# Optimization experiments

Hardware: AMD Instinct MI355X
Metric: run time of the kernel (lower is better)

The kernel has to match this reference:

```python
import jax, jax.numpy as jnp
import numpy as np

B, S, HID, H = 8, 128, 256, 4
DH = HID // H
FF = 4 * HID


def setup_inputs() -> dict:
    key = jax.random.key(0)
    ks = jax.random.split(key, 16)
    n = lambda i, shape: jax.random.normal(ks[i], shape, dtype=jnp.float32) * 0.02
    z = lambda shape: jnp.zeros(shape, dtype=jnp.float32)
    return dict(
        x=jax.random.normal(ks[0], (B, S, HID), dtype=jnp.float32),
        attention_mask=jnp.zeros((B, 1, S, S), dtype=jnp.float32),
        Wq=n(1, (HID, HID)), bq=z((HID,)),
        Wk=n(2, (HID, HID)), bk=z((HID,)),
        Wv=n(3, (HID, HID)), bv=z((HID,)),
        order_w=n(4, (2 * DH,)), order_b=z(()),
        dist_w=n(5, (2 * DH,)), dist_b=z(()),
        scalar=jax.random.normal(ks[6], (1,), dtype=jnp.float32),
        AWq=n(7, (HID, HID)), Abq=z((HID,)),
        AWk=n(8, (HID, HID)), Abk=z((HID,)),
        Wd=n(9, (HID, HID)), bd=z((HID,)),
        g1=jnp.ones((HID,), jnp.float32), beta1=z((HID,)),
        W1=n(10, (HID, FF)), b1=z((FF,)),
        W2=n(11, (FF, HID)), b2=z((HID,)),
        g2=jnp.ones((HID,), jnp.float32), beta2=z((HID,)),
    )


def _ln(t, g, b, eps=1e-12):
    m = t.mean(-1, keepdims=True)
    v = ((t - m) ** 2).mean(-1, keepdims=True)
    return (t - m) / jnp.sqrt(v + eps) * g + b


def _heads(t):
    # [B,S,HID] -> [B,H,S,DH]
    return t.reshape(B, S, H, DH).transpose(0, 2, 1, 3)


def reference(x, attention_mask, Wq, bq, Wk, bk, Wv, bv, order_w, order_b,
              dist_w, dist_b, scalar, AWq, Abq, AWk, Abk, Wd, bd,
              g1, beta1, W1, b1, W2, b2, g2, beta2):
    inv = 1.0 / jnp.sqrt(jnp.float32(DH))
    q = x @ Wq + bq
    k = x @ Wk + bk
    v = x @ Wv + bv
    qh, kh, vh = _heads(q), _heads(k), _heads(v)
    scores = jnp.einsum('bhqd,bhkd->bhqk', qh, kh)  # [B,H,S,S]

    # order/distance affines on concat(q_i, k_j): Linear(2*DH,1) decomposes into
    # per-token projections summed via broadcast (same math, no [B,H,S,S,2*DH] tensor)
    pr_order = jax.nn.sigmoid((qh @ order_w[:DH])[..., :, None]
                              + (kh @ order_w[DH:])[..., None, :] + order_b)
    gd_order = jnp.triu(jnp.ones((S, S), jnp.float32), k=1)
    err_order = (jnp.log(pr_order + 1e-24) * gd_order
                 + jnp.log(1.0 - pr_order + 1e-24) * (1.0 - gd_order))

    idx = jnp.arange(S)
    gd_dist = jnp.log(jnp.abs(idx[None, :] - idx[:, None]).astype(jnp.float32) + 1.0)
    pr_dist = ((qh @ dist_w[:DH])[..., :, None]
               + (kh @ dist_w[DH:])[..., None, :] + dist_b)
    err_dist = -jnp.square(gd_dist - pr_dist) * jnp.square(scalar[0]) * 0.5

    rich_scores = scores + err_order + err_dist
    softm = lambda s: jax.nn.softmax(s * inv + attention_mask, axis=-1)
    rich_probs = softm(rich_scores)
    origin_probs = softm(scores)

    # rich/calibrated combine ('fixed'): softmax(origin + 0.5 * rich)
    combined = jax.nn.softmax(origin_probs + 0.5 * rich_probs, axis=-1)

    # two-level attack attention on transformed mixed q/k
    aq, ak = _heads(q @ AWq + Abq), _heads(k @ AWk + Abk)
    attack_probs = softm(jnp.einsum('bhqd,bhkd->bhqk', aq, ak))
    final_probs = jax.nn.softmax(combined + 0.5 * attack_probs, axis=-1)

    ctx = jnp.einsum('bhqk,bhkd->bhqd', final_probs, vh)
    ctx = ctx.transpose(0, 2, 1, 3).reshape(B, S, HID)
    h = _ln(ctx @ Wd + bd + x, g1, beta1)
    f = jax.nn.gelu(h @ W1 + b1, approximate=False) @ W2 + b2
    return _ln(f + h, g2, beta2)
```

## Files before the change

kernel.cpp:

```cpp
#include <hip/hip_runtime.h>
#include <math.h>

#define B_  8
#define S_  128
#define HID_ 256
#define H_  4
#define DH_ 64
#define FF_ 1024
#define M_  (B_ * S_)

typedef _Float16 half_t;
typedef __attribute__((ext_vector_type(8))) _Float16 half8;
typedef __attribute__((ext_vector_type(4))) float floatx4;

enum { EP_F32 = 0, EP_F16 = 1, EP_F16B = 2, EP_GELU = 3, EP_PROJ = 4 };

__device__ __forceinline__ floatx4 mfma16(half8 a, half8 b, floatx4 c) {
    return __builtin_amdgcn_mfma_f32_16x16x32_f16(a, b, c, 0, 0, 0);
}

__device__ __forceinline__ float qred_sum(float v) {
#pragma unroll
    for (int o = 1; o < 16; o <<= 1) v += __shfl_xor(v, o, 64);
    return v;
}
__device__ __forceinline__ float wred64(float v) {
#pragma unroll
    for (int o = 1; o < 64; o <<= 1) v += __shfl_xor(v, o, 64);
    return v;
}
__device__ __forceinline__ void sm8(float (&v)[8]) {
    float s = 0.f;
#pragma unroll
    for (int j = 0; j < 8; ++j) { v[j] = __expf(v[j]); s += v[j]; }
    s = qred_sum(s);
    float r = 1.f / s;
#pragma unroll
    for (int j = 0; j < 8; ++j) v[j] *= r;
}

template<int EPI, int KLEN>
__device__ __forceinline__ void mgemm(
    half8 (&Asf)[2][4][64], half8 (&Bsf)[2][4][64],
    const half_t* __restrict__ A, int ldA,
    const half_t* __restrict__ Bt, int ldB,
    int m0, int n0,
    const float* __restrict__ bias,
    float* __restrict__ Cf, half_t* __restrict__ Ch, int ldC,
    const float* __restrict__ pw1, const float* __restrict__ pw2,
    float* __restrict__ po1, float* __restrict__ po2, int hsel,
    int tidp)
{
    constexpr int kt = KLEN >> 5;
    const int w = tidp >> 6, l = tidp & 63;
    const int sr = tidp >> 2;
    const int sq = tidp & 3;
    const int sdst = (sr & 15) | (sq << 4);
    const int smt = sr >> 4;
    const half_t* Ap = A + (size_t)(m0 + sr) * ldA + sq * 8;
    const half_t* Bp = Bt + (size_t)(n0 + sr) * ldB + sq * 8;

    half8 ra[kt], rb[kt];
#pragma unroll
    for (int t = 0; t < kt; ++t) {
        ra[t] = *(const half8*)(Ap + t * 32);
        rb[t] = *(const half8*)(Bp + t * 32);
    }

    floatx4 zero = {0.f, 0.f, 0.f, 0.f};
    floatx4 acc[4] = {zero, zero, zero, zero};

    Asf[0][smt][sdst] = ra[0];
    Bsf[0][smt][sdst] = rb[0];
    __syncthreads();
#pragma unroll
    for (int t = 0; t < kt; ++t) {
        const int buf = t & 1;
        half8 a = Asf[buf][w][l];
        acc[0] = mfma16(a, Bsf[buf][0][l], acc[0]);
        acc[1] = mfma16(a, Bsf[buf][1][l], acc[1]);
        acc[2] = mfma16(a, Bsf[buf][2][l], acc[2]);
        acc[3] = mfma16(a, Bsf[buf][3][l], acc[3]);
        if (t + 1 < kt) {
            Asf[buf ^ 1][smt][sdst] = ra[t + 1];
            Bsf[buf ^ 1][smt][sdst] = rb[t + 1];
            __syncthreads();
        }
    }

    const int quad = l >> 4, lc = l & 15;
    const int rowb = m0 + w * 16 + quad * 4;
    float bvv[4] = {0.f, 0.f, 0.f, 0.f};
    if (EPI >= EP_F16B) {
#pragma unroll
        for (int nt = 0; nt < 4; ++nt) bvv[nt] = bias[n0 + nt * 16 + lc];
    }
    float pw1v[4], pw2v[4];
    if (EPI == EP_PROJ) {
#pragma unroll
        for (int nt = 0; nt < 4; ++nt) {
            pw1v[nt] = pw1[nt * 16 + lc];
            pw2v[nt] = pw2[nt * 16 + lc];
        }
    }
#pragma unroll
    for (int rr = 0; rr < 4; ++rr) {
        float ov[4];
#pragma unroll
        for (int nt = 0; nt < 4; ++nt) {
            float o = acc[nt][rr];
            if (EPI >= EP_F16B) o += bvv[nt];
            if (EPI == EP_GELU) o = 0.5f * o * (1.f + erff(o * 0.70710678118654752f));
            ov[nt] = o;
            const size_t ci = (size_t)(rowb + rr) * ldC + n0 + nt * 16 + lc;
            if (EPI == EP_F32) Cf[ci] = o;
            else Ch[ci] = (half_t)o;
        }
        if (EPI == EP_PROJ) {
            float po = ov[0] * pw1v[0] + ov[1] * pw1v[1] + ov[2] * pw1v[2] + ov[3] * pw1v[3];
            float pd = ov[0] * pw2v[0] + ov[1] * pw2v[1] + ov[2] * pw2v[2] + ov[3] * pw2v[3];
#pragma unroll
            for (int off = 1; off < 16; off <<= 1) {
                po += __shfl_xor(po, off, 64);
                pd += __shfl_xor(pd, off, 64);
            }
            if (lc == 0) {
                const int m = rowb + rr;
                const int idx = ((m >> 7) * H_ + hsel) * S_ + (m & 127);
                po1[idx] = po;
                po2[idx] = pd;
            }
        }
    }
}

__global__ __launch_bounds__(256) void prep_kernel(
    const float* __restrict__ x,
    const float* __restrict__ Wq, const float* __restrict__ Wk,
    const float* __restrict__ Wv, const float* __restrict__ Wd,
    const float* __restrict__ W1, const float* __restrict__ W2,
    const float* __restrict__ AWq, const float* __restrict__ AWk,
    const float* __restrict__ bq, const float* __restrict__ bk,
    const float* __restrict__ Abq, const float* __restrict__ Abk,
    half_t* __restrict__ x16, half_t* __restrict__ WqT, half_t* __restrict__ WkT,
    half_t* __restrict__ WvT, half_t* __restrict__ WdT,
    half_t* __restrict__ W1T, half_t* __restrict__ W2T,
    half_t* __restrict__ WcqT, half_t* __restrict__ WckT,
    float* __restrict__ bcq, float* __restrict__ bck)
{
    __shared__ union {
        half_t tl[64][72];
        struct { half_t As[64][264]; half_t Bs[64][264]; } c;
        float red[4][64];
    } sm;
    const int tid = threadIdx.x;
    const int j = blockIdx.x;

    if (j < 256) {
        const int base = j * 1024 + tid * 4;
        float4 vv = *(const float4*)(x + base);
        x16[base + 0] = (half_t)vv.x;
        x16[base + 1] = (half_t)vv.y;
        x16[base + 2] = (half_t)vv.z;
        x16[base + 3] = (half_t)vv.w;
        return;
    }
    if (j < 448) {
        int t = j - 256;
        const float* src; half_t* dst; int K, N, k0, n0;
        if (t < 64) {
            int m = t >> 4, q = t & 15;
            const float* ins[4] = {Wq, Wk, Wv, Wd};
            half_t* outs[4] = {WqT, WkT, WvT, WdT};
            src = ins[m]; dst = outs[m]; K = 256; N = 256;
            k0 = (q & 3) * 64; n0 = (q >> 2) * 64;
        } else if (t < 128) {
            int q = t - 64; src = W1; dst = W1T; K = 256; N = 1024;
            k0 = (q & 3) * 64; n0 = (q >> 2) * 64;
        } else {
            int q = t - 128; src = W2; dst = W2T; K = 1024; N = 256;
            k0 = (q >> 2) * 64; n0 = (q & 3) * 64;
        }
        const int r = tid >> 2, c0 = (tid & 3) * 16;
#pragma unroll 4
        for (int i = 0; i < 16; ++i)
            sm.tl[c0 + i][r] = (half_t)src[(size_t)(k0 + r) * N + n0 + c0 + i];
        __syncthreads();
#pragma unroll 4
        for (int i = 0; i < 16; ++i)
            dst[(size_t)(n0 + r) * K + k0 + c0 + i] = sm.tl[r][c0 + i];
        return;
    }
    if (j < 480) {
        int t = j - 448;
        const int z = t >> 4, q = t & 15;
        const int m0 = (q >> 2) * 64, n0 = (q & 3) * 64;
        const float* AW = z ? AWk : AWq;
        const float* W  = z ? Wk : Wq;
        half_t* C       = z ? WckT : WcqT;
        {
            const float* srcA = AW + (size_t)tid * HID_ + m0;
#pragma unroll 4
            for (int i = 0; i < 16; ++i) {
                float4 v = *(const float4*)(srcA + i * 4);
                sm.c.As[i * 4 + 0][tid] = (half_t)v.x;
                sm.c.As[i * 4 + 1][tid] = (half_t)v.y;
                sm.c.As[i * 4 + 2][tid] = (half_t)v.z;
                sm.c.As[i * 4 + 3][tid] = (half_t)v.w;
            }
        }
        {
            const int bn = tid >> 2, bc = (tid & 3) * 64;
            const float* srcB = W + (size_t)(n0 + bn) * HID_ + bc;
            half_t* dstB = &sm.c.Bs[bn][bc];
#pragma unroll 4
            for (int i = 0; i < 16; ++i) {
                float4 v = *(const float4*)(srcB + i * 4);
                dstB[i * 4 + 0] = (half_t)v.x;
                dstB[i * 4 + 1] = (half_t)v.y;
                dstB[i * 4 + 2] = (half_t)v.z;
                dstB[i * 4 + 3] = (half_t)v.w;
            }
        }
        __syncthreads();
        const int w = tid >> 6, l = tid & 63;
        const int quad = l >> 4, lc = l & 15;
        const floatx4 zero = {0.f, 0.f, 0.f, 0.f};
        floatx4 acc[4] = {zero, zero, zero, zero};
#pragma unroll
        for (int kt = 0; kt < 8; ++kt) {
            half8 a = *(const half8*)&sm.c.As[w * 16 + lc][kt * 32 + quad * 8];
#pragma unroll
            for (int nt = 0; nt < 4; ++nt) {
                half8 b = *(const half8*)&sm.c.Bs[nt * 16 + lc][kt * 32 + quad * 8];
                acc[nt] = mfma16(a, b, acc[nt]);
            }
        }
#pragma unroll
        for (int nt = 0; nt < 4; ++nt)
#pragma unroll
            for (int rr = 0; rr < 4; ++rr)
                C[(size_t)(m0 + w * 16 + quad * 4 + rr) * HID_ + n0 + nt * 16 + lc] =
                    (half_t)acc[nt][rr];
        return;
    }
    {
        int t = j - 480;
        const int z = t >> 2, xb = t & 3;
        const float* bsrc = z ? bk : bq;
        const float* AW   = z ? AWk : AWq;
        const float* Ab   = z ? Abk : Abq;
        float* bco        = z ? bck : bcq;
        int l = tid & 63, kc = tid >> 6;
        int n = xb * 64 + l;
        float p = 0.f;
#pragma unroll 8
        for (int kk = 0; kk < 64; ++kk) {
            int k = kc * 64 + kk;
            p = fmaf(bsrc[k], AW[(size_t)k * HID_ + n], p);
        }
        sm.red[kc][l] = p;
        __syncthreads();
        if (kc == 0)
            bco[n] = sm.red[0][l] + sm.red[1][l] + sm.red[2][l] + sm.red[3][l] + Ab[n];
    }
}

__global__ __launch_bounds__(256) void xgemm5(
    const half_t* __restrict__ x16,
    const half_t* __restrict__ WqT, const float* __restrict__ bq,
    const half_t* __restrict__ WkT, const float* __restrict__ bk,
    const half_t* __restrict__ WvT, const float* __restrict__ bv,
    const half_t* __restrict__ WcqT, const float* __restrict__ bcq,
    const half_t* __restrict__ WckT, const float* __restrict__ bck,
    const float* __restrict__ order_w, const float* __restrict__ dist_w,
    half_t* __restrict__ q16, half_t* __restrict__ k16, half_t* __restrict__ v16,
    half_t* __restrict__ aq16, half_t* __restrict__ ak16,
    float* __restrict__ qoA, float* __restrict__ qdA,
    float* __restrict__ koA, float* __restrict__ kdA)
{
    __shared__ half8 Asf[2][4][64], Bsf[2][4][64];
    const int j = blockIdx.x;
    const int z = j >> 6, q = j & 63;
    const int m0 = (q >> 2) * 64, n0 = (q & 3) * 64, bx = q & 3;
    if (z == 0)
        mgemm<EP_PROJ, 256>(Asf, Bsf, x16, HID_, WqT, HID_, m0, n0,
                            bq, nullptr, q16, HID_, order_w, dist_w, qoA, qdA, bx,
                            threadIdx.x);
    else if (z == 1)
        mgemm<EP_PROJ, 256>(Asf, Bsf, x16, HID_, WkT, HID_, m0, n0,
                            bk, nullptr, k16, HID_, order_w + DH_, dist_w + DH_,
                            koA, kdA, bx, threadIdx.x);
    else if (z == 2)
        mgemm<EP_F16B, 256>(Asf, Bsf, x16, HID_, WvT, HID_, m0, n0,
                            bv, nullptr, v16, HID_, nullptr, nullptr, nullptr, nullptr, 0,
                            threadIdx.x);
    else if (z == 3)
        mgemm<EP_F16B, 256>(Asf, Bsf, x16, HID_, WcqT, HID_, m0, n0,
                            bcq, nullptr, aq16, HID_, nullptr, nullptr, nullptr, nullptr, 0,
                            threadIdx.x);
    else
        mgemm<EP_F16B, 256>(Asf, Bsf, x16, HID_, WckT, HID_, m0, n0,
                            bck, nullptr, ak16, HID_, nullptr, nullptr, nullptr, nullptr, 0,
                            threadIdx.x);
}

__global__ __launch_bounds__(64) void attn_kernel(
    const half_t* __restrict__ q16, const half_t* __restrict__ k16,
    const half_t* __restrict__ v16, const half_t* __restrict__ aq16,
    const half_t* __restrict__ ak16,
    const float* __restrict__ qoA, const float* __restrict__ qdA,
    const float* __restrict__ koA, const float* __restrict__ kdA,
    const float* __restrict__ mask,
    const float* __restrict__ order_b_p, const float* __restrict__ dist_b_p,
    const float* __restrict__ scalar_p,
    half_t* __restrict__ ctx16)
{
    __shared__ half8 Kf[2][8][64], AKf[2][8][64];
    __shared__ half_t Vt[64][136];
    __shared__ half_t Pm[16][136];

    const int l = threadIdx.x;
    const int quad = l >> 4, lc = l & 15;
    const int bh = blockIdx.x >> 3, rt = blockIdx.x & 7;
    const int b = bh >> 2, h = bh & 3;
    const size_t hoff = (size_t)b * S_ * HID_ + (size_t)h * DH_;

#pragma unroll
    for (int u = 0; u < 16; ++u) {
        int idx = u * 64 + l;
        int j = idx >> 3, c = idx & 7;
        size_t g = hoff + (size_t)j * HID_ + c * 8;
        int kt = c >> 2, jt = j >> 4, sl = (j & 15) | ((c & 3) << 4);
        Kf[kt][jt][sl]  = *(const half8*)(k16 + g);
        AKf[kt][jt][sl] = *(const half8*)(ak16 + g);
    }
#pragma unroll
    for (int u = 0; u < 16; ++u) {
        int j = (u >> 3) * 64 + l;
        int c = u & 7;
        half8 vv = *(const half8*)(v16 + hoff + (size_t)j * HID_ + c * 8);
#pragma unroll
        for (int e = 0; e < 8; ++e) Vt[c * 8 + e][j] = vv[e];
    }
    __syncthreads();

    half8 qf[2], aqf[2];
#pragma unroll
    for (int kt = 0; kt < 2; ++kt) {
        size_t g = hoff + (size_t)(rt * 16 + lc) * HID_ + kt * 32 + quad * 8;
        qf[kt]  = *(const half8*)(q16 + g);
        aqf[kt] = *(const half8*)(aq16 + g);
    }
    floatx4 zero = {0.f, 0.f, 0.f, 0.f};
    floatx4 accS[8], accA[8];
#pragma unroll
    for (int jt = 0; jt < 8; ++jt) { accS[jt] = zero; accA[jt] = zero; }
#pragma unroll
    for (int kt = 0; kt < 2; ++kt) {
#pragma unroll
        for (int jt = 0; jt < 8; ++jt) {
            accS[jt] = mfma16(qf[kt], Kf[kt][jt][l], accS[jt]);
            accA[jt] = mfma16(aqf[kt], AKf[kt][jt][l], accA[jt]);
        }
    }

    const float ob = order_b_p[0], db = dist_b_p[0];
    const float scl = scalar_p[0];
    const float s2 = scl * scl;
    const float inv = 0.125f;
    float kov[8], kdv[8];
#pragma unroll
    for (int jt = 0; jt < 8; ++jt) {
        kov[jt] = koA[bh * S_ + jt * 16 + lc];
        kdv[jt] = kdA[bh * S_ + jt * 16 + lc];
    }
#pragma unroll
    for (int reg = 0; reg < 4; ++reg) {
        const int il = quad * 4 + reg;
        const int i  = rt * 16 + il;
        float qo = qoA[bh * S_ + i], qd = qdA[bh * S_ + i];
        const float* mrow = mask + ((size_t)(b * S_ + i)) * S_;
        float mk[8], lg[8], as_[8];
#pragma unroll
        for (int jt = 0; jt < 8; ++jt) {
            mk[jt] = mrow[jt * 16 + lc];
            lg[jt] = accS[jt][reg];
            as_[jt] = accA[jt][reg];
        }
        float p0[8];
#pragma unroll
        for (int jt = 0; jt < 8; ++jt) p0[jt] = lg[jt] * inv + mk[jt];
        sm8(p0);
        float p1[8];
#pragma unroll
        for (int jt = 0; jt < 8; ++jt) {
            int j = jt * 16 + lc;
            float pr = 1.f / (1.f + __expf(-(qo + kov[jt] + ob)));
            float sel = (j > i) ? pr : 1.f - pr;
            float erro = __logf(sel + 1e-24f);
            float gd = __logf(fabsf((float)(j - i)) + 1.f);
            float dd = gd - (qd + kdv[jt] + db);
            p1[jt] = (lg[jt] + erro - 0.5f * dd * dd * s2) * inv + mk[jt];
        }
        sm8(p1);
#pragma unroll
        for (int jt = 0; jt < 8; ++jt) p0[jt] += 0.5f * p1[jt];
        sm8(p0);
#pragma unroll
        for (int jt = 0; jt < 8; ++jt) p1[jt] = as_[jt] * inv + mk[jt];
        sm8(p1);
#pragma unroll
        for (int jt = 0; jt < 8; ++jt) p0[jt] += 0.5f * p1[jt];
        sm8(p0);
#pragma unroll
        for (int jt = 0; jt < 8; ++jt) Pm[il][jt * 16 + lc] = (half_t)p0[jt];
    }
    __syncthreads();

    half8 pa_[4];
#pragma unroll
    for (int kt = 0; kt < 4; ++kt)
        pa_[kt] = *(const half8*)&Pm[lc][kt * 32 + quad * 8];
    floatx4 apv[4];
#pragma unroll
    for (int nt = 0; nt < 4; ++nt) apv[nt] = zero;
#pragma unroll
    for (int nt = 0; nt < 4; ++nt) {
#pragma unroll
        for (int kt = 0; kt < 4; ++kt) {
            half8 vf = *(const half8*)&Vt[nt * 16 + lc][kt * 32 + quad * 8];
            apv[nt] = mfma16(pa_[kt], vf, apv[nt]);
        }
    }
#pragma unroll
    for (int nt = 0; nt < 4; ++nt) {
#pragma unroll
        for (int reg = 0; reg < 4; ++reg) {
            int i = rt * 16 + quad * 4 + reg;
            ctx16[hoff + (size_t)i * HID_ + nt * 16 + lc] = (half_t)apv[nt][reg];
        }
    }
}

__global__ __launch_bounds__(512) void dense_ln1_kernel(
    const half_t* __restrict__ ctx16, const half_t* __restrict__ WdT,
    const float* __restrict__ x, const float* __restrict__ bd,
    const float* __restrict__ g1, const float* __restrict__ beta1,
    float* __restrict__ hb32, half_t* __restrict__ h16)
{
    __shared__ half8 Af[8][64];
    __shared__ float hS[16][257];
    const int tid = threadIdx.x;
    const int r0 = blockIdx.x * 16;
    const int w = tid >> 6, l = tid & 63;
    const int quad = l >> 4, lc = l & 15;
    const floatx4 zero = {0.f, 0.f, 0.f, 0.f};

    {
        int row = tid >> 5, c = tid & 31;
        Af[c >> 2][row | ((c & 3) << 4)] =
            *(const half8*)(ctx16 + (size_t)(r0 + row) * HID_ + c * 8);
    }
    __syncthreads();

    {
        const int n0 = w * 32;
        half8 bw[8][2];
#pragma unroll
        for (int kt = 0; kt < 8; ++kt)
#pragma unroll
            for (int nt = 0; nt < 2; ++nt)
                bw[kt][nt] = *(const half8*)(WdT + (size_t)(n0 + nt * 16 + lc) * HID_
                                             + kt * 32 + quad * 8);
        floatx4 acc[2] = {zero, zero};
#pragma unroll
        for (int kt = 0; kt < 8; ++kt) {
            half8 a = Af[kt][l];
            acc[0] = mfma16(a, bw[kt][0], acc[0]);
            acc[1] = mfma16(a, bw[kt][1], acc[1]);
        }
#pragma unroll
        for (int nt = 0; nt < 2; ++nt)
#pragma unroll
            for (int rr = 0; rr < 4; ++rr) {
                int row = quad * 4 + rr, col = n0 + nt * 16 + lc;
                hS[row][col] = acc[nt][rr] + bd[col]
                             + x[(size_t)(r0 + row) * HID_ + col];
            }
    }
    __syncthreads();

    {
        const int row = tid >> 5, jj = tid & 31;
        float s = 0.f;
#pragma unroll
        for (int i = 0; i < 8; ++i) s += hS[row][i * 32 + jj];
#pragma unroll
        for (int o = 1; o < 32; o <<= 1) s += __shfl_xor(s, o, 64);
        float mean = s * (1.f / 256.f);
        float vs = 0.f;
#pragma unroll
        for (int i = 0; i < 8; ++i) { float d = hS[row][i * 32 + jj] - mean; vs += d * d; }
#pragma unroll
        for (int o = 1; o < 32; o <<= 1) vs += __shfl_xor(vs, o, 64);
        float rs = rsqrtf(vs * (1.f / 256.f) + 1e-12f);
#pragma unroll
        for (int i = 0; i < 8; ++i) {
            int col = i * 32 + jj;
            float v = (hS[row][col] - mean) * rs * g1[col] + beta1[col];
            size_t gi = (size_t)(r0 + row) * HID_ + col;
            hb32[gi] = v;
            h16[gi] = (half_t)v;
        }
    }
}

__global__ __launch_bounds__(256) void ff1_kernel(
    const half_t* __restrict__ h16, const half_t* __restrict__ W1T,
    const float* __restrict__ b1, half_t* __restrict__ f116)
{
    __shared__ half8 Asf[2][4][64], Bsf[2][4][64];
    const int j = blockIdx.x;
    mgemm<EP_GELU, 256>(Asf, Bsf, h16, HID_, W1T, HID_,
                        (j >> 4) * 64, (j & 15) * 64,
                        b1, nullptr, f116, FF_, nullptr, nullptr, nullptr, nullptr, 0,
                        threadIdx.x);
}

__global__ __launch_bounds__(256) void ff2_kernel(
    const half_t* __restrict__ f116, const half_t* __restrict__ W2T,
    float* __restrict__ pf0, float* __restrict__ pf1)
{
    __shared__ half8 Asf[2][4][64], Bsf[2][4][64];
    const int j = blockIdx.x;
    const int m0 = (j >> 3) * 64, n0 = ((j >> 1) & 3) * 64, ks = j & 1;
    float* C = ks ? pf1 : pf0;
    mgemm<EP_F32, 512>(Asf, Bsf, f116 + ks * 512, FF_, W2T + ks * 512, FF_,
                       m0, n0,
                       nullptr, C, nullptr, HID_, nullptr, nullptr, nullptr, nullptr, 0,
                       threadIdx.x);
}

__global__ __launch_bounds__(256) void ln2_kernel(
    const float* __restrict__ pf0, const float* __restrict__ pf1,
    const float* __restrict__ b2, const float* __restrict__ hb32,
    const float* __restrict__ g2, const float* __restrict__ beta2,
    float* __restrict__ out)
{
    const int tid = threadIdx.x;
    const int row = blockIdx.x * 4 + (tid >> 6);
    const int jj = tid & 63;
    const size_t base = (size_t)row * HID_;
    float v[4];
    float s = 0.f;
#pragma unroll
    for (int i = 0; i < 4; ++i) {
        int col = i * 64 + jj;
        v[i] = pf0[base + col] + pf1[base + col] + b2[col] + hb32[base + col];
        s += v[i];
    }
    s = wred64(s);
    float mean = s * (1.f / 256.f);
    float vs = 0.f;
#pragma unroll
    for (int i = 0; i < 4; ++i) { float d = v[i] - mean; vs += d * d; }
    vs = wred64(vs);
    float rs = rsqrtf(vs * (1.f / 256.f) + 1e-12f);
#pragma unroll
    for (int i = 0; i < 4; ++i) {
        int col = i * 64 + jj;
        out[base + col] = (v[i] - mean) * rs * g2[col] + beta2[col];
    }
}

extern "C" void kernel_launch(void* const* d_in, const int* in_sizes, int n_in,
                              void* d_out, int out_size, void* d_ws, size_t ws_size,
                              hipStream_t stream) {
    const float* x        = (const float*)d_in[0];
    const float* mask     = (const float*)d_in[1];
    const float* Wq       = (const float*)d_in[2];
    const float* bq       = (const float*)d_in[3];
    const float* Wk       = (const float*)d_in[4];
    const float* bk       = (const float*)d_in[5];
    const float* Wv       = (const float*)d_in[6];
    const float* bv       = (const float*)d_in[7];
    const float* order_w  = (const float*)d_in[8];
    const float* order_b  = (const float*)d_in[9];
    const float* dist_w   = (const float*)d_in[10];
    const float* dist_b   = (const float*)d_in[11];
    const float* scalar   = (const float*)d_in[12];
    const float* AWq      = (const float*)d_in[13];
    const float* Abq      = (const float*)d_in[14];
    const float* AWk      = (const float*)d_in[15];
    const float* Abk      = (const float*)d_in[16];
    const float* Wd       = (const float*)d_in[17];
    const float* bd       = (const float*)d_in[18];
    const float* g1       = (const float*)d_in[19];
    const float* beta1    = (const float*)d_in[20];
    const float* W1       = (const float*)d_in[21];
    const float* b1       = (const float*)d_in[22];
    const float* W2       = (const float*)d_in[23];
    const float* b2       = (const float*)d_in[24];
    const float* g2       = (const float*)d_in[25];
    const float* beta2    = (const float*)d_in[26];

    float* ws = (float*)d_ws;
    size_t off = 0;
    auto ahf = [&](size_t nh) { half_t* p = (half_t*)(ws + off); off += nh / 2; return p; };
    auto afl = [&](size_t n) { float* p = ws + off; off += n; return p; };

    half_t* x16   = ahf(M_ * HID_);
    half_t* WqT   = ahf(HID_ * HID_);
    half_t* WkT   = ahf(HID_ * HID_);
    half_t* WvT   = ahf(HID_ * HID_);
    half_t* WdT   = ahf(HID_ * HID_);
    half_t* W1T   = ahf(HID_ * FF_);
    half_t* W2T   = ahf(HID_ * FF_);
    half_t* WcqT  = ahf(HID_ * HID_);
    half_t* WckT  = ahf(HID_ * HID_);
    half_t* q16   = ahf(M_ * HID_);
    half_t* k16   = ahf(M_ * HID_);
    half_t* v16   = ahf(M_ * HID_);
    half_t* aq16  = ahf(M_ * HID_);
    half_t* ak16  = ahf(M_ * HID_);
    half_t* ctx16 = ahf(M_ * HID_);
    half_t* h16   = ahf(M_ * HID_);
    half_t* f116  = ahf(M_ * FF_);
    float* hb32 = afl(M_ * HID_);
    float* pf0  = afl(M_ * HID_);
    float* pf1  = afl(M_ * HID_);
    float* bcq  = afl(256);
    float* bck  = afl(256);
    float* qoA  = afl(B_ * H_ * S_);
    float* qdA  = afl(B_ * H_ * S_);
    float* koA  = afl(B_ * H_ * S_);
    float* kdA  = afl(B_ * H_ * S_);

    prep_kernel<<<488, 256, 0, stream>>>(
        x, Wq, Wk, Wv, Wd, W1, W2, AWq, AWk, bq, bk, Abq, Abk,
        x16, WqT, WkT, WvT, WdT, W1T, W2T, WcqT, WckT, bcq, bck);
    xgemm5<<<320, 256, 0, stream>>>(
        x16, WqT, bq, WkT, bk, WvT, bv, WcqT, bcq, WckT, bck, order_w, dist_w,
        q16, k16, v16, aq16, ak16, qoA, qdA, koA, kdA);
    attn_kernel<<<256, 64, 0, stream>>>(
        q16, k16, v16, aq16, ak16, qoA, qdA, koA, kdA,
        mask, order_b, dist_b, scalar, ctx16);
    dense_ln1_kernel<<<64, 512, 0, stream>>>(
        ctx16, WdT, x, bd, g1, beta1, hb32, h16);
    ff1_kernel<<<256, 256, 0, stream>>>(h16, W1T, b1, f116);
    ff2_kernel<<<128, 256, 0, stream>>>(f116, W2T, pf0, pf1);
    ln2_kernel<<<256, 256, 0, stream>>>(pf0, pf1, b2, hb32, g2, beta2, (float*)d_out);
}
```

Measured before the change: 153.3 us.

## Defer Wd/W1/W2 transposes into projection GEMM launch and widen attention loads

Moves the fp16 conversion of the Wd, W1 and W2 weights out of the prep kernel and into extra blocks of the QKV projection launch. This shortens the critical prep stage and lets that work overlap with the projection GEMMs. The x conversion now uses fewer blocks that each convert 16 elements per thread. The attention kernel goes from 64 to 256 threads so K/AK/V staging into shared memory is spread across four waves, after which three waves exit and one wave does the compute. The now-redundant barrier before the Pm readback is removed because only one wave remains.

After: 155.8 us. About the same (+1.6%).

```diff
diff --git a/kernel.cpp b/kernel.cpp
--- a/kernel.cpp
+++ b/kernel.cpp
@@ -137,14 +137,12 @@
 __global__ __launch_bounds__(256) void prep_kernel(
     const float* __restrict__ x,
     const float* __restrict__ Wq, const float* __restrict__ Wk,
-    const float* __restrict__ Wv, const float* __restrict__ Wd,
-    const float* __restrict__ W1, const float* __restrict__ W2,
+    const float* __restrict__ Wv,
     const float* __restrict__ AWq, const float* __restrict__ AWk,
     const float* __restrict__ bq, const float* __restrict__ bk,
     const float* __restrict__ Abq, const float* __restrict__ Abk,
     half_t* __restrict__ x16, half_t* __restrict__ WqT, half_t* __restrict__ WkT,
-    half_t* __restrict__ WvT, half_t* __restrict__ WdT,
-    half_t* __restrict__ W1T, half_t* __restrict__ W2T,
+    half_t* __restrict__ WvT,
     half_t* __restrict__ WcqT, half_t* __restrict__ WckT,
     float* __restrict__ bcq, float* __restrict__ bck)
 {
@@ -156,43 +154,37 @@
     const int tid = threadIdx.x;
     const int j = blockIdx.x;
 
-    if (j < 256) {
-        const int base = j * 1024 + tid * 4;
-        float4 vv = *(const float4*)(x + base);
-        x16[base + 0] = (half_t)vv.x;
-        x16[base + 1] = (half_t)vv.y;
-        x16[base + 2] = (half_t)vv.z;
-        x16[base + 3] = (half_t)vv.w;
+    if (j < 64) {
+        const int base = j * 4096 + tid * 16;
+#pragma unroll
+        for (int p = 0; p < 4; ++p) {
+            float4 vv = *(const float4*)(x + base + p * 4);
+            x16[base + p * 4 + 0] = (half_t)vv.x;
+            x16[base + p * 4 + 1] = (half_t)vv.y;
+            x16[base + p * 4 + 2] = (half_t)vv.z;
+            x16[base + p * 4 + 3] = (half_t)vv.w;
+        }
         return;
     }
-    if (j < 448) {
-        int t = j - 256;
-        const float* src; half_t* dst; int K, N, k0, n0;
-        if (t < 64) {
-            int m = t >> 4, q = t & 15;
-            const float* ins[4] = {Wq, Wk, Wv, Wd};
-            half_t* outs[4] = {WqT, WkT, WvT, WdT};
-            src = ins[m]; dst = outs[m]; K = 256; N = 256;
-            k0 = (q & 3) * 64; n0 = (q >> 2) * 64;
-        } else if (t < 128) {
-            int q = t - 64; src = W1; dst = W1T; K = 256; N = 1024;
-            k0 = (q & 3) * 64; n0 = (q >> 2) * 64;
-        } else {
-            int q = t - 128; src = W2; dst = W2T; K = 1024; N = 256;
-            k0 = (q >> 2) * 64; n0 = (q & 3) * 64;
-        }
+    if (j < 112) {
+        int t = j - 64;
+        int m = t >> 4, q = t & 15;
+        const float* ins[3] = {Wq, Wk, Wv};
+        half_t* outs[3] = {WqT, WkT, WvT};
+        const float* src = ins[m]; half_t* dst = outs[m];
+        const int k0 = (q & 3) * 64, n0 = (q >> 2) * 64;
         const int r = tid >> 2, c0 = (tid & 3) * 16;
 #pragma unroll 4
         for (int i = 0; i < 16; ++i)
-            sm.tl[c0 + i][r] = (half_t)src[(size_t)(k0 + r) * N + n0 + c0 + i];
+            sm.tl[c0 + i][r] = (half_t)src[(size_t)(k0 + r) * HID_ + n0 + c0 + i];
         __syncthreads();
 #pragma unroll 4
         for (int i = 0; i < 16; ++i)
-            dst[(size_t)(n0 + r) * K + k0 + c0 + i] = sm.tl[r][c0 + i];
+            dst[(size_t)(n0 + r) * HID_ + k0 + c0 + i] = sm.tl[r][c0 + i];
         return;
     }
-    if (j < 480) {
-        int t = j - 448;
+    if (j < 144) {
+        int t = j - 112;
         const int z = t >> 4, q = t & 15;
         const int m0 = (q >> 2) * 64, n0 = (q & 3) * 64;
         const float* AW = z ? AWk : AWq;
@@ -245,7 +237,7 @@
         return;
     }
     {
-        int t = j - 480;
+        int t = j - 144;
         const int z = t >> 2, xb = t & 3;
         const float* bsrc = z ? bk : bq;
         const float* AW   = z ? AWk : AWq;
@@ -277,35 +269,65 @@
     half_t* __restrict__ q16, half_t* __restrict__ k16, half_t* __restrict__ v16,
     half_t* __restrict__ aq16, half_t* __restrict__ ak16,
     float* __restrict__ qoA, float* __restrict__ qdA,
-    float* __restrict__ koA, float* __restrict__ kdA)
-{
-    __shared__ half8 Asf[2][4][64], Bsf[2][4][64];
+    float* __restrict__ koA, float* __restrict__ kdA,
+    const float* __restrict__ Wd, const float* __restrict__ W1,
+    const float* __restrict__ W2,
+    half_t* __restrict__ WdT, half_t* __restrict__ W1T, half_t* __restrict__ W2T)
+{
+    __shared__ union {
+        struct { half8 Asf[2][4][64]; half8 Bsf[2][4][64]; } g;
+        half_t tl[64][72];
+    } sm;
     const int j = blockIdx.x;
-    const int z = j >> 6, q = j & 63;
-    const int m0 = (q >> 2) * 64, n0 = (q & 3) * 64, bx = q & 3;
-    if (z == 0)
-        mgemm<EP_PROJ, 256>(Asf, Bsf, x16, HID_, WqT, HID_, m0, n0,
-                            bq, nullptr, q16, HID_, order_w, dist_w, qoA, qdA, bx,
-                            threadIdx.x);
-    else if (z == 1)
-        mgemm<EP_PROJ, 256>(Asf, Bsf, x16, HID_, WkT, HID_, m0, n0,
-                            bk, nullptr, k16, HID_, order_w + DH_, dist_w + DH_,
-                            koA, kdA, bx, threadIdx.x);
-    else if (z == 2)
-        mgemm<EP_F16B, 256>(Asf, Bsf, x16, HID_, WvT, HID_, m0, n0,
-                            bv, nullptr, v16, HID_, nullptr, nullptr, nullptr, nullptr, 0,
-                            threadIdx.x);
-    else if (z == 3)
-        mgemm<EP_F16B, 256>(Asf, Bsf, x16, HID_, WcqT, HID_, m0, n0,
-                            bcq, nullptr, aq16, HID_, nullptr, nullptr, nullptr, nullptr, 0,
-                            threadIdx.x);
-    else
-        mgemm<EP_F16B, 256>(Asf, Bsf, x16, HID_, WckT, HID_, m0, n0,
-                            bck, nullptr, ak16, HID_, nullptr, nullptr, nullptr, nullptr, 0,
-                            threadIdx.x);
-}
-
-__global__ __launch_bounds__(64) void attn_kernel(
+    if (j < 320) {
+        const int z = j >> 6, q = j & 63;
+        const int m0 = (q >> 2) * 64, n0 = (q & 3) * 64, bx = q & 3;
+        if (z == 0)
+            mgemm<EP_PROJ, 256>(sm.g.Asf, sm.g.Bsf, x16, HID_, WqT, HID_, m0, n0,
+                                bq, nullptr, q16, HID_, order_w, dist_w, qoA, qdA, bx,
+                                threadIdx.x);
+        else if (z == 1)
+            mgemm<EP_PROJ, 256>(sm.g.Asf, sm.g.Bsf, x16, HID_, WkT, HID_, m0, n0,
+                                bk, nullptr, k16, HID_, order_w + DH_, dist_w + DH_,
+                                koA, kdA, bx, threadIdx.x);
+        else if (z == 2)
+            mgemm<EP_F16B, 256>(sm.g.Asf, sm.g.Bsf, x16, HID_, WvT, HID_, m0, n0,
+                                bv, nullptr, v16, HID_, nullptr, nullptr, nullptr, nullptr, 0,
+                                threadIdx.x);
+        else if (z == 3)
+            mgemm<EP_F16B, 256>(sm.g.Asf, sm.g.Bsf, x16, HID_, WcqT, HID_, m0, n0,
+                                bcq, nullptr, aq16, HID_, nullptr, nullptr, nullptr, nullptr, 0,
+                                threadIdx.x);
+        else
+            mgemm<EP_F16B, 256>(sm.g.Asf, sm.g.Bsf, x16, HID_, WckT, HID_, m0, n0,
+                                bck, nullptr, ak16, HID_, nullptr, nullptr, nullptr, nullptr, 0,
+                                threadIdx.x);
+        return;
+    }
+    int t = j - 320;
+    const float* src; half_t* dst; int K, N, k0, n0;
+    if (t < 16) {
+        src = Wd; dst = WdT; K = 256; N = 256;
+        k0 = (t & 3) * 64; n0 = (t >> 2) * 64;
+    } else if (t < 80) {
+        int q = t - 16; src = W1; dst = W1T; K = 256; N = 1024;
+        k0 = (q & 3) * 64; n0 = (q >> 2) * 64;
+    } else {
+        int q = t - 80; src = W2; dst = W2T; K = 1024; N = 256;
+        k0 = (q >> 2) * 64; n0 = (q & 3) * 64;
+    }
+    const int tid = threadIdx.x;
+    const int r = tid >> 2, c0 = (tid & 3) * 16;
+#pragma unroll 4
+    for (int i = 0; i < 16; ++i)
+        sm.tl[c0 + i][r] = (half_t)src[(size_t)(k0 + r) * N + n0 + c0 + i];
+    __syncthreads();
+#pragma unroll 4
+    for (int i = 0; i < 16; ++i)
+        dst[(size_t)(n0 + r) * K + k0 + c0 + i] = sm.tl[r][c0 + i];
+}
+
+__global__ __launch_bounds__(256) void attn_kernel(
     const half_t* __restrict__ q16, const half_t* __restrict__ k16,
     const half_t* __restrict__ v16, const half_t* __restrict__ aq16,
     const half_t* __restrict__ ak16,
@@ -320,15 +342,16 @@
     __shared__ half_t Vt[64][136];
     __shared__ half_t Pm[16][136];
 
-    const int l = threadIdx.x;
+    const int tid = threadIdx.x;
+    const int w = tid >> 6, l = tid & 63;
     const int quad = l >> 4, lc = l & 15;
     const int bh = blockIdx.x >> 3, rt = blockIdx.x & 7;
     const int b = bh >> 2, h = bh & 3;
     const size_t hoff = (size_t)b * S_ * HID_ + (size_t)h * DH_;
 
 #pragma unroll
-    for (int u = 0; u < 16; ++u) {
-        int idx = u * 64 + l;
+    for (int u = 0; u < 4; ++u) {
+        int idx = u * 256 + tid;
         int j = idx >> 3, c = idx & 7;
         size_t g = hoff + (size_t)j * HID_ + c * 8;
         int kt = c >> 2, jt = j >> 4, sl = (j & 15) | ((c & 3) << 4);
@@ -336,14 +359,15 @@
         AKf[kt][jt][sl] = *(const half8*)(ak16 + g);
     }
 #pragma unroll
-    for (int u = 0; u < 16; ++u) {
-        int j = (u >> 3) * 64 + l;
-        int c = u & 7;
+    for (int u = 0; u < 4; ++u) {
+        int idx = u * 256 + tid;
+        int j = idx >> 3, c = idx & 7;
         half8 vv = *(const half8*)(v16 + hoff + (size_t)j * HID_ + c * 8);
 #pragma unroll
         for (int e = 0; e < 8; ++e) Vt[c * 8 + e][j] = vv[e];
     }
     __syncthreads();
+    if (w != 0) return;
 
     half8 qf[2], aqf[2];
 #pragma unroll
@@ -416,8 +440,6 @@
 #pragma unroll
         for (int jt = 0; jt < 8; ++jt) Pm[il][jt * 16 + lc] = (half_t)p0[jt];
     }
-    __syncthreads();
-
     half8 pa_[4];
 #pragma unroll
     for (int kt = 0; kt < 4; ++kt)
@@ -637,13 +659,14 @@
     float* koA  = afl(B_ * H_ * S_);
     float* kdA  = afl(B_ * H_ * S_);
 
-    prep_kernel<<<488, 256, 0, stream>>>(
-        x, Wq, Wk, Wv, Wd, W1, W2, AWq, AWk, bq, bk, Abq, Abk,
-        x16, WqT, WkT, WvT, WdT, W1T, W2T, WcqT, WckT, bcq, bck);
-    xgemm5<<<320, 256, 0, stream>>>(
+    prep_kernel<<<152, 256, 0, stream>>>(
+        x, Wq, Wk, Wv, AWq, AWk, bq, bk, Abq, Abk,
+        x16, WqT, WkT, WvT, WcqT, WckT, bcq, bck);
+    xgemm5<<<464, 256, 0, stream>>>(
         x16, WqT, bq, WkT, bk, WvT, bv, WcqT, bcq, WckT, bck, order_w, dist_w,
-        q16, k16, v16, aq16, ak16, qoA, qdA, koA, kdA);
-    attn_kernel<<<256, 64, 0, stream>>>(
+        q16, k16, v16, aq16, ak16, qoA, qdA, koA, kdA,
+        Wd, W1, W2, WdT, W1T, W2T);
+    attn_kernel<<<256, 256, 0, stream>>>(
         q16, k16, v16, aq16, ak16, qoA, qdA, koA, kdA,
         mask, order_b, dist_b, scalar, ctx16);
     dense_ln1_kernel<<<64, 512, 0, stream>>>(
```
